# Performance work log

Hardware: AMD Instinct MI355X
Metric: run time of the kernel (lower is better)

## Reference

```python
import jax, jax.numpy as jnp
import numpy as np

B, H, L, D, S = 4, 16, 4096, 64, 128

def setup_inputs() -> dict:
    key = jax.random.key(0)
    k1, k2 = jax.random.split(key)
    x = jax.random.normal(k1, (B, H, L, D), dtype=jnp.float32)
    c = jax.random.normal(k2, (H, S, D), dtype=jnp.float32)
    # codebook rows are unit-normalized at init (matches torch init)
    c = c / jnp.linalg.norm(c, axis=-1, keepdims=True)
    return {"x": x, "c": c}

def reference(x, c):
    # cosine-similarity scores: [B,H,L,S]
    cos_sim = jnp.einsum('bhld,hsd->bhls', x, c)
    delta_index = jnp.argmax(cos_sim, axis=-1)            # [B,H,L]
    delta_onehot = jax.nn.one_hot(delta_index, c.shape[-2], dtype=jnp.float32)  # [B,H,L,S]
    return (delta_onehot, c)
```

## Files before the change

### kernel.cpp

```cpp
#include <hip/hip_runtime.h>
#include <hip/hip_bf16.h>
#include <math.h>

constexpr int BB = 4;
constexpr int HH = 16;
constexpr int LL = 4096;
constexpr int DD = 64;
constexpr int SS = 128;


__global__ __launch_bounds__(256) void quantizer_kernel(
    const float* __restrict__ x,
    const float* __restrict__ c,
    float* __restrict__ out,
    float* __restrict__ out_c)
{
    const int tid = threadIdx.x;
    const int blk = blockIdx.x;
    const long long row0 = (long long)blk * 256;
    const long long r = row0 + tid;

    const int h = (int)((row0 >> 12) & (HH - 1));
    const float* __restrict__ chead = c + (size_t)h * SS * DD;

    __shared__ float4 cb[SS * DD / 4];
    {
        const float4* __restrict__ csrc = (const float4*)chead;
        #pragma unroll
        for (int i = 0; i < 8; ++i)
            cb[tid + i * 256] = csrc[tid + i * 256];
    }

    float xr[DD];
    const float4* __restrict__ xp = (const float4*)(x + (size_t)r * DD);
    #pragma unroll
    for (int i = 0; i < DD / 4; ++i) {
        float4 v = xp[i];
        xr[4 * i + 0] = v.x;
        xr[4 * i + 1] = v.y;
        xr[4 * i + 2] = v.z;
        xr[4 * i + 3] = v.w;
    }

    __syncthreads();

    float best = -INFINITY;
    int bidx = 0;
    #pragma unroll 4
    for (int s = 0; s < SS; ++s) {
        const float4* __restrict__ crow = &cb[s * (DD / 4)];
        float a0 = 0.f, a1 = 0.f, a2 = 0.f, a3 = 0.f;
        #pragma unroll
        for (int d4 = 0; d4 < DD / 4; ++d4) {
            float4 cv = crow[d4];
            a0 = fmaf(xr[4 * d4 + 0], cv.x, a0);
            a1 = fmaf(xr[4 * d4 + 1], cv.y, a1);
            a2 = fmaf(xr[4 * d4 + 2], cv.z, a2);
            a3 = fmaf(xr[4 * d4 + 3], cv.w, a3);
        }
        float dot = (a0 + a1) + (a2 + a3);
        if (dot > best) { best = dot; bidx = s; }
    }

    __shared__ int amax[256];
    amax[tid] = bidx;
    __syncthreads();

    float4* __restrict__ op = (float4*)(out + (size_t)row0 * SS);
    #pragma unroll 4
    for (int i = tid; i < 8192; i += 256) {
        const int rr = i >> 5;
        const int s0 = (i & 31) * 4;
        const int am = amax[rr];
        float4 v;
        v.x = (s0 + 0 == am) ? 1.f : 0.f;
        v.y = (s0 + 1 == am) ? 1.f : 0.f;
        v.z = (s0 + 2 == am) ? 1.f : 0.f;
        v.w = (s0 + 3 == am) ? 1.f : 0.f;
        op[i] = v;
    }

    if (blk < 128) {
        const float4* __restrict__ src = (const float4*)c;
        float4* __restrict__ dst = (float4*)out_c;
        const int idx = blk * 256 + tid;
        dst[idx] = src[idx];
    }
}

extern "C" void kernel_launch(void* const* d_in, const int* in_sizes, int n_in,
                              void* d_out, int out_size, void* d_ws, size_t ws_size,
                              hipStream_t stream) {
    const float* x = (const float*)d_in[0];
    const float* c = (const float*)d_in[1];
    float* out = (float*)d_out;
    float* out_c = out + (size_t)BB * HH * LL * SS;

    const int rows = BB * HH * LL;
    const int blocks = rows / 256;
    quantizer_kernel<<<blocks, 256, 0, stream>>>(x, c, out, out_c);
}
```

Measured before the change: 248.2 us.

## Process two rows per thread and split codebook reads between LDS and global

Each thread now holds two x rows in registers, so every codebook element it loads feeds two dot products, and each block covers 512 rows. Only the first 56 codebook rows are staged in LDS; the other 72 are read straight from global memory through a vector-register offset, and the two paths are interleaved in one loop. The goal is to cut LDS read traffic per FMA and spread codebook loads across the LDS and vector-memory paths. In exchange, register pressure roughly doubles (launch bounds set to 2 waves), there are half as many blocks, and ties now explicitly resolve to the lower index.

```diff
diff --git a/kernel.cpp b/kernel.cpp
--- a/kernel.cpp
+++ b/kernel.cpp
@@ -8,8 +8,11 @@
 constexpr int DD = 64;
 constexpr int SS = 128;
 
+constexpr int S_LDS = 56;
+constexpr int S_VMEM = SS - S_LDS;
+constexpr int ROWS_PER_BLOCK = 512;
 
-__global__ __launch_bounds__(256) void quantizer_kernel(
+__global__ __launch_bounds__(256, 2) void quantizer_kernel(
     const float* __restrict__ x,
     const float* __restrict__ c,
     float* __restrict__ out,
@@ -17,58 +20,96 @@
 {
     const int tid = threadIdx.x;
     const int blk = blockIdx.x;
-    const long long row0 = (long long)blk * 256;
-    const long long r = row0 + tid;
-
+    const long long row0 = (long long)blk * ROWS_PER_BLOCK;
     const int h = (int)((row0 >> 12) & (HH - 1));
     const float* __restrict__ chead = c + (size_t)h * SS * DD;
 
-    __shared__ float4 cb[SS * DD / 4];
+    __shared__ float4 cb[S_LDS * DD / 4];
+    __shared__ int amax[ROWS_PER_BLOCK];
+
     {
         const float4* __restrict__ csrc = (const float4*)chead;
-        #pragma unroll
-        for (int i = 0; i < 8; ++i)
-            cb[tid + i * 256] = csrc[tid + i * 256];
+        for (int i = tid; i < S_LDS * DD / 4; i += 256)
+            cb[i] = csrc[i];
     }
 
-    float xr[DD];
-    const float4* __restrict__ xp = (const float4*)(x + (size_t)r * DD);
-    #pragma unroll
-    for (int i = 0; i < DD / 4; ++i) {
-        float4 v = xp[i];
-        xr[4 * i + 0] = v.x;
-        xr[4 * i + 1] = v.y;
-        xr[4 * i + 2] = v.z;
-        xr[4 * i + 3] = v.w;
+    float xa[DD], xb[DD];
+    {
+        const float4* __restrict__ xpA = (const float4*)(x + (size_t)(row0 + tid) * DD);
+        const float4* __restrict__ xpB = (const float4*)(x + (size_t)(row0 + 256 + tid) * DD);
+        #pragma unroll
+        for (int i = 0; i < DD / 4; ++i) {
+            float4 v = xpA[i];
+            xa[4*i+0] = v.x; xa[4*i+1] = v.y; xa[4*i+2] = v.z; xa[4*i+3] = v.w;
+            float4 w = xpB[i];
+            xb[4*i+0] = w.x; xb[4*i+1] = w.y; xb[4*i+2] = w.z; xb[4*i+3] = w.w;
+        }
     }
 
     __syncthreads();
 
-    float best = -INFINITY;
-    int bidx = 0;
-    #pragma unroll 4
-    for (int s = 0; s < SS; ++s) {
-        const float4* __restrict__ crow = &cb[s * (DD / 4)];
-        float a0 = 0.f, a1 = 0.f, a2 = 0.f, a3 = 0.f;
-        #pragma unroll
-        for (int d4 = 0; d4 < DD / 4; ++d4) {
-            float4 cv = crow[d4];
-            a0 = fmaf(xr[4 * d4 + 0], cv.x, a0);
-            a1 = fmaf(xr[4 * d4 + 1], cv.y, a1);
-            a2 = fmaf(xr[4 * d4 + 2], cv.z, a2);
-            a3 = fmaf(xr[4 * d4 + 3], cv.w, a3);
+    int vzero;
+    asm volatile("v_mov_b32 %0, 0" : "=v"(vzero));
+    const float4* __restrict__ cvm = (const float4*)chead + vzero;
+
+    float bestA = -INFINITY, bestB = -INFINITY;
+    int idxA = 0, idxB = 0;
+
+    auto upd = [](float& best, int& bidx, float d, int s) {
+        bool better = (d > best) || (d == best && s < bidx);
+        best = better ? d : best;
+        bidx = better ? s : bidx;
+    };
+
+    for (int i = 0; i < S_VMEM; ++i) {
+        {
+            const int s = S_LDS + i;
+            const float4* __restrict__ cr = cvm + s * (DD / 4);
+            float a0 = 0.f, a1 = 0.f, a2 = 0.f, a3 = 0.f;
+            float b0 = 0.f, b1 = 0.f, b2 = 0.f, b3 = 0.f;
+            #pragma unroll
+            for (int d4 = 0; d4 < DD / 4; ++d4) {
+                float4 cv = cr[d4];
+                a0 = fmaf(xa[4*d4+0], cv.x, a0);
+                a1 = fmaf(xa[4*d4+1], cv.y, a1);
+                a2 = fmaf(xa[4*d4+2], cv.z, a2);
+                a3 = fmaf(xa[4*d4+3], cv.w, a3);
+                b0 = fmaf(xb[4*d4+0], cv.x, b0);
+                b1 = fmaf(xb[4*d4+1], cv.y, b1);
+                b2 = fmaf(xb[4*d4+2], cv.z, b2);
+                b3 = fmaf(xb[4*d4+3], cv.w, b3);
+            }
+            upd(bestA, idxA, (a0 + a1) + (a2 + a3), s);
+            upd(bestB, idxB, (b0 + b1) + (b2 + b3), s);
         }
-        float dot = (a0 + a1) + (a2 + a3);
-        if (dot > best) { best = dot; bidx = s; }
+        if (i < S_LDS) {
+            const float4* __restrict__ cr = &cb[i * (DD / 4)];
+            float a0 = 0.f, a1 = 0.f, a2 = 0.f, a3 = 0.f;
+            float b0 = 0.f, b1 = 0.f, b2 = 0.f, b3 = 0.f;
+            #pragma unroll
+            for (int d4 = 0; d4 < DD / 4; ++d4) {
+                float4 cv = cr[d4];
+                a0 = fmaf(xa[4*d4+0], cv.x, a0);
+                a1 = fmaf(xa[4*d4+1], cv.y, a1);
+                a2 = fmaf(xa[4*d4+2], cv.z, a2);
+                a3 = fmaf(xa[4*d4+3], cv.w, a3);
+                b0 = fmaf(xb[4*d4+0], cv.x, b0);
+                b1 = fmaf(xb[4*d4+1], cv.y, b1);
+                b2 = fmaf(xb[4*d4+2], cv.z, b2);
+                b3 = fmaf(xb[4*d4+3], cv.w, b3);
+            }
+            upd(bestA, idxA, (a0 + a1) + (a2 + a3), i);
+            upd(bestB, idxB, (b0 + b1) + (b2 + b3), i);
+        }
     }
 
-    __shared__ int amax[256];
-    amax[tid] = bidx;
+    amax[tid] = idxA;
+    amax[tid + 256] = idxB;
     __syncthreads();
 
     float4* __restrict__ op = (float4*)(out + (size_t)row0 * SS);
     #pragma unroll 4
-    for (int i = tid; i < 8192; i += 256) {
+    for (int i = tid; i < ROWS_PER_BLOCK * (SS / 4); i += 256) {
         const int rr = i >> 5;
         const int s0 = (i & 31) * 4;
         const int am = amax[rr];
@@ -97,6 +138,6 @@
     float* out_c = out + (size_t)BB * HH * LL * SS;
 
     const int rows = BB * HH * LL;
-    const int blocks = rows / 256;
+    const int blocks = rows / ROWS_PER_BLOCK;
     quantizer_kernel<<<blocks, 256, 0, stream>>>(x, c, out, out_c);
 }
```

Result: slower. 719.6 us (+189.9%).

## Split codebook reads between LDS and per-lane global loads to balance bandwidth

Applied to the files above, without the earlier changes.

Only the first 64 codebook rows are staged in LDS. The other 64 rows are read directly from global memory through a per-lane (VGPR-offset) pointer, so the compiler issues vector loads rather than scalar loads. The loop interleaves one LDS row and one global row so both memory paths run at once, which halves LDS traffic and footprint. The change also adds an occupancy hint to the launch bounds and an explicit lowest-index tie-break for the argmax. The risk is extra global/L1 traffic and register pressure under the new bound.

```diff
diff --git a/kernel.cpp b/kernel.cpp
--- a/kernel.cpp
+++ b/kernel.cpp
@@ -8,8 +8,10 @@
 constexpr int DD = 64;
 constexpr int SS = 128;
 
+constexpr int S_LDS = 64;
+constexpr int S_VMEM = SS - S_LDS;
 
-__global__ __launch_bounds__(256) void quantizer_kernel(
+__global__ __launch_bounds__(256, 4) void quantizer_kernel(
     const float* __restrict__ x,
     const float* __restrict__ c,
     float* __restrict__ out,
@@ -23,46 +25,72 @@
     const int h = (int)((row0 >> 12) & (HH - 1));
     const float* __restrict__ chead = c + (size_t)h * SS * DD;
 
-    __shared__ float4 cb[SS * DD / 4];
+    __shared__ float4 cb[S_LDS * DD / 4];
+    __shared__ int amax[256];
+
     {
         const float4* __restrict__ csrc = (const float4*)chead;
         #pragma unroll
-        for (int i = 0; i < 8; ++i)
+        for (int i = 0; i < S_LDS * DD / 4 / 256; ++i)
             cb[tid + i * 256] = csrc[tid + i * 256];
     }
 
     float xr[DD];
-    const float4* __restrict__ xp = (const float4*)(x + (size_t)r * DD);
-    #pragma unroll
-    for (int i = 0; i < DD / 4; ++i) {
-        float4 v = xp[i];
-        xr[4 * i + 0] = v.x;
-        xr[4 * i + 1] = v.y;
-        xr[4 * i + 2] = v.z;
-        xr[4 * i + 3] = v.w;
+    {
+        const float4* __restrict__ xp = (const float4*)(x + (size_t)r * DD);
+        #pragma unroll
+        for (int i = 0; i < DD / 4; ++i) {
+            float4 v = xp[i];
+            xr[4*i+0] = v.x; xr[4*i+1] = v.y; xr[4*i+2] = v.z; xr[4*i+3] = v.w;
+        }
     }
 
     __syncthreads();
 
+    int vzero;
+    asm volatile("v_mov_b32 %0, 0" : "=v"(vzero));
+    const float4* __restrict__ cvm = (const float4*)chead + vzero;
+
     float best = -INFINITY;
     int bidx = 0;
-    #pragma unroll 4
-    for (int s = 0; s < SS; ++s) {
-        const float4* __restrict__ crow = &cb[s * (DD / 4)];
-        float a0 = 0.f, a1 = 0.f, a2 = 0.f, a3 = 0.f;
-        #pragma unroll
-        for (int d4 = 0; d4 < DD / 4; ++d4) {
-            float4 cv = crow[d4];
-            a0 = fmaf(xr[4 * d4 + 0], cv.x, a0);
-            a1 = fmaf(xr[4 * d4 + 1], cv.y, a1);
-            a2 = fmaf(xr[4 * d4 + 2], cv.z, a2);
-            a3 = fmaf(xr[4 * d4 + 3], cv.w, a3);
+
+    auto upd = [&](float d, int s) {
+        bool better = (d > best) || (d == best && s < bidx);
+        best = better ? d : best;
+        bidx = better ? s : bidx;
+    };
+
+    #pragma unroll 2
+    for (int i = 0; i < S_LDS; ++i) {
+        {
+            const int s = S_LDS + i;
+            const float4* __restrict__ cr = cvm + s * (DD / 4);
+            float a0 = 0.f, a1 = 0.f, a2 = 0.f, a3 = 0.f;
+            #pragma unroll
+            for (int d4 = 0; d4 < DD / 4; ++d4) {
+                float4 cv = cr[d4];
+                a0 = fmaf(xr[4*d4+0], cv.x, a0);
+                a1 = fmaf(xr[4*d4+1], cv.y, a1);
+                a2 = fmaf(xr[4*d4+2], cv.z, a2);
+                a3 = fmaf(xr[4*d4+3], cv.w, a3);
+            }
+            upd((a0 + a1) + (a2 + a3), s);
         }
-        float dot = (a0 + a1) + (a2 + a3);
-        if (dot > best) { best = dot; bidx = s; }
+        {
+            const float4* __restrict__ cr = &cb[i * (DD / 4)];
+            float a0 = 0.f, a1 = 0.f, a2 = 0.f, a3 = 0.f;
+            #pragma unroll
+            for (int d4 = 0; d4 < DD / 4; ++d4) {
+                float4 cv = cr[d4];
+                a0 = fmaf(xr[4*d4+0], cv.x, a0);
+                a1 = fmaf(xr[4*d4+1], cv.y, a1);
+                a2 = fmaf(xr[4*d4+2], cv.z, a2);
+                a3 = fmaf(xr[4*d4+3], cv.w, a3);
+            }
+            upd((a0 + a1) + (a2 + a3), i);
+        }
     }
 
-    __shared__ int amax[256];
     amax[tid] = bidx;
     __syncthreads();
 
```

New measurement: 310.1 us. 24.9% more time.
